# Performance work log

Hardware: AMD Instinct MI355X
Metric: run time of the kernel (lower is better)

## Reference

```python
import jax, jax.numpy as jnp
import numpy as np


def setup_inputs() -> dict:
    key = jax.random.key(0)
    k1, k2 = jax.random.split(key)
    x = jax.random.normal(k1, (16, 2048, 512), dtype=jnp.float32)
    embed = jax.random.normal(k2, (4096, 512), dtype=jnp.float32)
    return {"x": x, "embed": embed}


def reference(x, embed):
    # encode: flatten leading dims, compute -||x - e||^2 via expansion, argmax
    shape = x.shape
    xf = x.reshape(-1, shape[-1])                       # [N, d]
    x_sq = jnp.sum(xf * xf, axis=1, keepdims=True)      # [N, 1]
    e_sq = jnp.sum(embed * embed, axis=1)[None, :]      # [1, K]
    dist = -(x_sq - 2.0 * (xf @ embed.T) + e_sq)        # [N, K]
    embed_ind = jnp.argmax(dist, axis=-1)               # [N]
    embed_ind = embed_ind.reshape(shape[:-1])           # [B, S]
    # decode: embedding lookup (dequantize)
    quantize = embed[embed_ind]                         # [B, S, d]
    return embed_ind, quantize
```

## Files before the change

kernel.cpp:

```cpp
#include <hip/hip_runtime.h>
#include <hip/hip_fp16.h>
#include <stdint.h>


typedef _Float16 f16;
typedef __attribute__((ext_vector_type(4))) _Float16 f16x4;
typedef __attribute__((ext_vector_type(8))) _Float16 f16x8;
typedef __attribute__((ext_vector_type(4))) float f32x4;

#define DDIM 512
#define KCODES 4096
#define NSPLIT 2
#define BM 256
#define BN 256
#define BK 32
#define NCH ((KCODES / NSPLIT) / BN)
#define NSTEPS (NCH * (DDIM / BK))
#define PSTRIDE (NSPLIT * 2)

__device__ __forceinline__ void gload_lds16(const void* g, void* l) {
  __builtin_amdgcn_global_load_lds(
      (const __attribute__((address_space(1))) void*)g,
      (__attribute__((address_space(3))) void*)l,
      16, 0, 0);
}

__global__ void convert_split(const float* __restrict__ in,
                              f16* __restrict__ hi, f16* __restrict__ lo, int n4) {
  int stride = gridDim.x * blockDim.x;
  for (int i = blockIdx.x * blockDim.x + threadIdx.x; i < n4; i += stride) {
    float4 v = ((const float4*)in)[i];
    float vv[4] = {v.x, v.y, v.z, v.w};
    f16x4 h, l;
#pragma unroll
    for (int j = 0; j < 4; ++j) {
      _Float16 hh = (_Float16)vv[j];
      h[j] = hh;
      l[j] = (_Float16)(vv[j] - (float)hh);
    }
    ((f16x4*)hi)[i] = h;
    ((f16x4*)lo)[i] = l;
  }
}

__global__ void esq_kernel(const float* __restrict__ e, float* __restrict__ esq) {
  int gw = (blockIdx.x * blockDim.x + threadIdx.x) >> 6;
  int lane = threadIdx.x & 63;
  if (gw >= KCODES) return;
  const float4* row = (const float4*)(e + (size_t)gw * DDIM);
  float4 a = row[lane * 2];
  float4 b = row[lane * 2 + 1];
  double s = (double)a.x * a.x + (double)a.y * a.y + (double)a.z * a.z + (double)a.w * a.w +
             (double)b.x * b.x + (double)b.y * b.y + (double)b.z * b.z + (double)b.w * b.w;
#pragma unroll
  for (int m = 32; m; m >>= 1) s += __shfl_xor(s, m, 64);
  if (lane == 0) esq[gw] = (float)s;
}

__global__ __launch_bounds__(512, 2) void vq_main(
    const f16* __restrict__ Ah, const f16* __restrict__ Al,
    const f16* __restrict__ Bh, const f16* __restrict__ Bl,
    const float* __restrict__ esq, float2* __restrict__ partials, int nRowBlocks) {
  __shared__ char lds[131072];
  __shared__ float esqLds[KCODES / NSPLIT];

  int nwg = gridDim.x;
  int bid = blockIdx.x;
  int cpx = nwg >> 3;
  int swz = (bid & 7) * cpx + (bid >> 3);
  int nsp = swz / nRowBlocks;
  int brow = swz % nRowBlocks;
  int rowbase = brow * BM;

  int tid = threadIdx.x;
  int lane = tid & 63;
  int wv = tid >> 6;
  int wr = wv >> 1, wc = wv & 1;
  int l15 = lane & 15, lg = lane >> 4;

  const int aoff = (wr * 64 + l15) * 64 + lg * 16;
  const int boff = (wc * 128 + l15) * 64 + lg * 16;

  int srow = tid >> 2;
  int skoff = (tid & 3) * 8;
  const int codesPer = KCODES / NSPLIT;

  const f16* aSrcH = Ah + (size_t)(rowbase + srow) * DDIM + skoff;
  const f16* aSrcL = Al + (size_t)(rowbase + srow) * DDIM + skoff;
  const f16* bBaseH = Bh + (size_t)(nsp * codesPer + srow) * DDIM + skoff;
  const f16* bBaseL = Bl + (size_t)(nsp * codesPer + srow) * DDIM + skoff;

  auto STAGE = [&](int buf, int ch, int kk) {
    char* base = lds + buf * 65536 + wv * 1024;
    size_t bo = (size_t)(ch * BN) * DDIM + kk;
    gload_lds16(aSrcH + kk, base);
    gload_lds16(aSrcH + kk + (size_t)128 * DDIM, base + 8192);
    gload_lds16(aSrcL + kk, base + 16384);
    gload_lds16(aSrcL + kk + (size_t)128 * DDIM, base + 16384 + 8192);
    gload_lds16(bBaseH + bo, base + 32768);
    gload_lds16(bBaseH + bo + (size_t)128 * DDIM, base + 32768 + 8192);
    gload_lds16(bBaseL + bo, base + 49152);
    gload_lds16(bBaseL + bo + (size_t)128 * DDIM, base + 49152 + 8192);
  };

  float bestv[16];
  int besti[16];
#pragma unroll
  for (int t = 0; t < 16; ++t) { bestv[t] = -3.4e38f; besti[t] = 0; }

  f32x4 acc[4][8];

  {
    float4 ev = ((const float4*)(esq + nsp * codesPer))[tid];
    ((float4*)esqLds)[tid] = make_float4(0.5f * ev.x, 0.5f * ev.y, 0.5f * ev.z, 0.5f * ev.w);
  }
  STAGE(0, 0, 0);
  __syncthreads();

#pragma unroll 1
  for (int s = 0; s < NSTEPS; ++s) {
    int cur = s & 1;
    int ch = s >> 4;
    int ns = s + 1;
    if (ns < NSTEPS) {
      STAGE(cur ^ 1, ns >> 4, (ns & 15) * BK);
      asm volatile("s_waitcnt vmcnt(8)" ::: "memory");
    } else {
      asm volatile("s_waitcnt vmcnt(0)" ::: "memory");
    }
    __builtin_amdgcn_s_barrier();
    __builtin_amdgcn_sched_barrier(0);

    if ((s & 15) == 0) {
#pragma unroll
      for (int i = 0; i < 4; ++i)
#pragma unroll
        for (int j = 0; j < 8; ++j) acc[i][j] = (f32x4){0.f, 0.f, 0.f, 0.f};
    }

    char* base = lds + cur * 65536;
    f16x8 ah[4], al[4], bh[8], bl[8];
#pragma unroll
    for (int i = 0; i < 4; ++i) ah[i] = *(const f16x8*)(base + aoff + i * 1024);
#pragma unroll
    for (int j = 0; j < 8; ++j) bh[j] = *(const f16x8*)(base + 32768 + boff + j * 1024);
    __builtin_amdgcn_s_setprio(1);
#pragma unroll
    for (int i = 0; i < 4; ++i)
#pragma unroll
      for (int j = 0; j < 8; ++j)
        acc[i][j] = __builtin_amdgcn_mfma_f32_16x16x32_f16(ah[i], bh[j], acc[i][j], 0, 0, 0);
    __builtin_amdgcn_s_setprio(0);
#pragma unroll
    for (int i = 0; i < 4; ++i) al[i] = *(const f16x8*)(base + 16384 + aoff + i * 1024);
    __builtin_amdgcn_s_setprio(1);
#pragma unroll
    for (int i = 0; i < 4; ++i)
#pragma unroll
      for (int j = 0; j < 8; ++j)
        acc[i][j] = __builtin_amdgcn_mfma_f32_16x16x32_f16(al[i], bh[j], acc[i][j], 0, 0, 0);
    __builtin_amdgcn_s_setprio(0);
#pragma unroll
    for (int j = 0; j < 8; ++j) bl[j] = *(const f16x8*)(base + 49152 + boff + j * 1024);
    __builtin_amdgcn_s_setprio(1);
#pragma unroll
    for (int i = 0; i < 4; ++i)
#pragma unroll
      for (int j = 0; j < 8; ++j)
        acc[i][j] = __builtin_amdgcn_mfma_f32_16x16x32_f16(ah[i], bl[j], acc[i][j], 0, 0, 0);
    __builtin_amdgcn_s_setprio(0);

    if ((s & 15) == 15) {
      int cloc = ch * BN + wc * 128;
#pragma unroll
      for (int j = 0; j < 8; ++j) {
        float eh = esqLds[cloc + j * 16 + l15];
        int code = nsp * codesPer + cloc + j * 16 + l15;
#pragma unroll
        for (int i = 0; i < 4; ++i)
#pragma unroll
          for (int r = 0; r < 4; ++r) {
            float v = acc[i][j][r] - eh;
            int t = i * 4 + r;
            if (v > bestv[t]) { bestv[t] = v; besti[t] = code; }
          }
      }
    }
    __builtin_amdgcn_sched_barrier(0);
    __builtin_amdgcn_s_barrier();
  }

#pragma unroll
  for (int m = 1; m < 16; m <<= 1) {
#pragma unroll
    for (int t = 0; t < 16; ++t) {
      float ov = __shfl_xor(bestv[t], m, 64);
      int oi = __shfl_xor(besti[t], m, 64);
      if (ov > bestv[t] || (ov == bestv[t] && oi < besti[t])) { bestv[t] = ov; besti[t] = oi; }
    }
  }
  if (l15 == 0) {
#pragma unroll
    for (int i = 0; i < 4; ++i)
#pragma unroll
      for (int r = 0; r < 4; ++r) {
        int row = rowbase + wr * 64 + i * 16 + lg * 4 + r;
        partials[(size_t)row * PSTRIDE + nsp * 2 + wc] =
            make_float2(bestv[i * 4 + r], (float)besti[i * 4 + r]);
      }
  }
}

__global__ void reduce_decode(const float* __restrict__ embed,
                              const float2* __restrict__ partials,
                              float* __restrict__ outIdx, float* __restrict__ outQ,
                              int nRows) {
  int gw = (blockIdx.x * blockDim.x + threadIdx.x) >> 6;
  int lane = threadIdx.x & 63;
  if (gw >= nRows) return;
  float bv = -3.4e38f;
  int bi = 0x7fffffff;
#pragma unroll
  for (int s = 0; s < PSTRIDE; ++s) {
    float2 p = partials[(size_t)gw * PSTRIDE + s];
    int idx = (int)p.y;
    if (p.x > bv || (p.x == bv && idx < bi)) { bv = p.x; bi = idx; }
  }
  if (lane == 0) outIdx[gw] = (float)bi;
  const float4* src = (const float4*)(embed + (size_t)bi * DDIM);
  float4* dst = (float4*)(outQ + (size_t)gw * DDIM);
  dst[lane] = src[lane];
  dst[lane + 64] = src[lane + 64];
}

extern "C" void kernel_launch(void* const* d_in, const int* in_sizes, int n_in,
                              void* d_out, int out_size, void* d_ws, size_t ws_size,
                              hipStream_t stream) {
  const float* x = (const float*)d_in[0];
  const float* embed = (const float*)d_in[1];
  int nX = in_sizes[0];
  int nRows = nX / DDIM;
  int nRowBlocks = nRows / BM;

  float* out = (float*)d_out;
  float* outIdx = out;
  float* outQ = out + nRows;

  size_t szA = (size_t)nRows * DDIM * sizeof(f16);
  size_t szB = (size_t)KCODES * DDIM * sizeof(f16);
  size_t szEsq = (size_t)KCODES * sizeof(float);
  size_t szPart = (size_t)nRows * PSTRIDE * sizeof(float2);

  char* ws = (char*)d_ws;
  f16 *Ah, *Al, *Bh, *Bl;
  float* esq;
  float2* parts;
  size_t needFull = 2 * szA + 2 * szB + szEsq + szPart;
  if (ws_size >= needFull) {
    Ah = (f16*)ws;
    Al = (f16*)(ws + szA);
    Bh = (f16*)(ws + 2 * szA);
    Bl = (f16*)(ws + 2 * szA + szB);
    esq = (float*)(ws + 2 * szA + 2 * szB);
    parts = (float2*)(ws + 2 * szA + 2 * szB + szEsq);
  } else {
    Ah = (f16*)outQ;
    Al = Ah + (size_t)nRows * DDIM;
    Bh = (f16*)ws;
    Bl = (f16*)(ws + szB);
    esq = (float*)(ws + 2 * szB);
    parts = (float2*)(ws + 2 * szB + szEsq);
  }

  int n4x = nX / 4;
  int n4e = in_sizes[1] / 4;
  hipLaunchKernelGGL(convert_split, dim3(2048), dim3(256), 0, stream, x, Ah, Al, n4x);
  hipLaunchKernelGGL(convert_split, dim3((n4e + 255) / 256), dim3(256), 0, stream, embed, Bh, Bl, n4e);
  hipLaunchKernelGGL(esq_kernel, dim3(KCODES / 4), dim3(256), 0, stream, embed, esq);
  hipLaunchKernelGGL(vq_main, dim3(nRowBlocks * NSPLIT), dim3(512), 0, stream,
                     Ah, Al, Bh, Bl, esq, parts, nRowBlocks);
  hipLaunchKernelGGL(reduce_decode, dim3(nRows / 4), dim3(256), 0, stream,
                     embed, parts, outIdx, outQ, nRows);
}
```

Baseline: 410.8 us.

## Replace split-fp16 GEMM with single fp16 pass plus exact fixup of ambiguous rows

After: 1.061 ms. +158.2%, slower.

```diff
diff --git a/kernel.cpp b/kernel.cpp
--- a/kernel.cpp
+++ b/kernel.cpp
@@ -13,10 +13,10 @@
 #define NSPLIT 2
 #define BM 256
 #define BN 256
-#define BK 32
 #define NCH ((KCODES / NSPLIT) / BN)
-#define NSTEPS (NCH * (DDIM / BK))
+#define NSTEPS (NCH * (DDIM / 64))
 #define PSTRIDE (NSPLIT * 2)
+#define M_AMBIG 0.15f
 
 __device__ __forceinline__ void gload_lds16(const void* g, void* l) {
   __builtin_amdgcn_global_load_lds(
@@ -25,21 +25,14 @@
       16, 0, 0);
 }
 
-__global__ void convert_split(const float* __restrict__ in,
-                              f16* __restrict__ hi, f16* __restrict__ lo, int n4) {
+__global__ void convert_hi(const float* __restrict__ in, f16* __restrict__ hi, int n4) {
   int stride = gridDim.x * blockDim.x;
   for (int i = blockIdx.x * blockDim.x + threadIdx.x; i < n4; i += stride) {
     float4 v = ((const float4*)in)[i];
-    float vv[4] = {v.x, v.y, v.z, v.w};
-    f16x4 h, l;
-#pragma unroll
-    for (int j = 0; j < 4; ++j) {
-      _Float16 hh = (_Float16)vv[j];
-      h[j] = hh;
-      l[j] = (_Float16)(vv[j] - (float)hh);
-    }
+    f16x4 h;
+    h[0] = (_Float16)v.x; h[1] = (_Float16)v.y;
+    h[2] = (_Float16)v.z; h[3] = (_Float16)v.w;
     ((f16x4*)hi)[i] = h;
-    ((f16x4*)lo)[i] = l;
   }
 }
 
@@ -57,10 +50,11 @@
   if (lane == 0) esq[gw] = (float)s;
 }
 
-__global__ __launch_bounds__(512, 2) void vq_main(
-    const f16* __restrict__ Ah, const f16* __restrict__ Al,
-    const f16* __restrict__ Bh, const f16* __restrict__ Bl,
-    const float* __restrict__ esq, float2* __restrict__ partials, int nRowBlocks) {
+__global__ void zero_counter(int* c) { *c = 0; }
+
+__global__ __launch_bounds__(512, 2) void vq_approx(
+    const f16* __restrict__ Ah, const f16* __restrict__ Bh,
+    const float* __restrict__ esq, float4* __restrict__ partials, int nRowBlocks) {
   __shared__ char lds[131072];
   __shared__ float esqLds[KCODES / NSPLIT];
 
@@ -85,28 +79,26 @@
   int skoff = (tid & 3) * 8;
   const int codesPer = KCODES / NSPLIT;
 
-  const f16* aSrcH = Ah + (size_t)(rowbase + srow) * DDIM + skoff;
-  const f16* aSrcL = Al + (size_t)(rowbase + srow) * DDIM + skoff;
-  const f16* bBaseH = Bh + (size_t)(nsp * codesPer + srow) * DDIM + skoff;
-  const f16* bBaseL = Bl + (size_t)(nsp * codesPer + srow) * DDIM + skoff;
+  const f16* aSrc = Ah + (size_t)(rowbase + srow) * DDIM + skoff;
+  const f16* bBase = Bh + (size_t)(nsp * codesPer + srow) * DDIM + skoff;
 
   auto STAGE = [&](int buf, int ch, int kk) {
     char* base = lds + buf * 65536 + wv * 1024;
     size_t bo = (size_t)(ch * BN) * DDIM + kk;
-    gload_lds16(aSrcH + kk, base);
-    gload_lds16(aSrcH + kk + (size_t)128 * DDIM, base + 8192);
-    gload_lds16(aSrcL + kk, base + 16384);
-    gload_lds16(aSrcL + kk + (size_t)128 * DDIM, base + 16384 + 8192);
-    gload_lds16(bBaseH + bo, base + 32768);
-    gload_lds16(bBaseH + bo + (size_t)128 * DDIM, base + 32768 + 8192);
-    gload_lds16(bBaseL + bo, base + 49152);
-    gload_lds16(bBaseL + bo + (size_t)128 * DDIM, base + 49152 + 8192);
+    gload_lds16(aSrc + kk, base);
+    gload_lds16(aSrc + kk + (size_t)128 * DDIM, base + 8192);
+    gload_lds16(aSrc + kk + 32, base + 16384);
+    gload_lds16(aSrc + kk + 32 + (size_t)128 * DDIM, base + 16384 + 8192);
+    gload_lds16(bBase + bo, base + 32768);
+    gload_lds16(bBase + bo + (size_t)128 * DDIM, base + 32768 + 8192);
+    gload_lds16(bBase + bo + 32, base + 49152);
+    gload_lds16(bBase + bo + 32 + (size_t)128 * DDIM, base + 49152 + 8192);
   };
 
-  float bestv[16];
-  int besti[16];
-#pragma unroll
-  for (int t = 0; t < 16; ++t) { bestv[t] = -3.4e38f; besti[t] = 0; }
+  float v1[16], v2[16];
+  int i1[16];
+#pragma unroll
+  for (int t = 0; t < 16; ++t) { v1[t] = -3.4e38f; v2[t] = -3.4e38f; i1[t] = 0; }
 
   f32x4 acc[4][8];
 
@@ -120,18 +112,11 @@
 #pragma unroll 1
   for (int s = 0; s < NSTEPS; ++s) {
     int cur = s & 1;
-    int ch = s >> 4;
+    int ch = s >> 3;
     int ns = s + 1;
-    if (ns < NSTEPS) {
-      STAGE(cur ^ 1, ns >> 4, (ns & 15) * BK);
-      asm volatile("s_waitcnt vmcnt(8)" ::: "memory");
-    } else {
-      asm volatile("s_waitcnt vmcnt(0)" ::: "memory");
-    }
-    __builtin_amdgcn_s_barrier();
-    __builtin_amdgcn_sched_barrier(0);
-
-    if ((s & 15) == 0) {
+    if (ns < NSTEPS) STAGE(cur ^ 1, ns >> 3, (ns & 7) * 64);
+
+    if ((s & 7) == 0) {
 #pragma unroll
       for (int i = 0; i < 4; ++i)
 #pragma unroll
@@ -139,38 +124,27 @@
     }
 
     char* base = lds + cur * 65536;
-    f16x8 ah[4], al[4], bh[8], bl[8];
-#pragma unroll
-    for (int i = 0; i < 4; ++i) ah[i] = *(const f16x8*)(base + aoff + i * 1024);
-#pragma unroll
-    for (int j = 0; j < 8; ++j) bh[j] = *(const f16x8*)(base + 32768 + boff + j * 1024);
-    __builtin_amdgcn_s_setprio(1);
+    f16x8 af[4], bf[8];
+#pragma unroll
+    for (int i = 0; i < 4; ++i) af[i] = *(const f16x8*)(base + aoff + i * 1024);
+#pragma unroll
+    for (int j = 0; j < 8; ++j) bf[j] = *(const f16x8*)(base + 32768 + boff + j * 1024);
 #pragma unroll
     for (int i = 0; i < 4; ++i)
 #pragma unroll
       for (int j = 0; j < 8; ++j)
-        acc[i][j] = __builtin_amdgcn_mfma_f32_16x16x32_f16(ah[i], bh[j], acc[i][j], 0, 0, 0);
-    __builtin_amdgcn_s_setprio(0);
-#pragma unroll
-    for (int i = 0; i < 4; ++i) al[i] = *(const f16x8*)(base + 16384 + aoff + i * 1024);
-    __builtin_amdgcn_s_setprio(1);
+        acc[i][j] = __builtin_amdgcn_mfma_f32_16x16x32_f16(af[i], bf[j], acc[i][j], 0, 0, 0);
+#pragma unroll
+    for (int i = 0; i < 4; ++i) af[i] = *(const f16x8*)(base + 16384 + aoff + i * 1024);
+#pragma unroll
+    for (int j = 0; j < 8; ++j) bf[j] = *(const f16x8*)(base + 49152 + boff + j * 1024);
 #pragma unroll
     for (int i = 0; i < 4; ++i)
 #pragma unroll
       for (int j = 0; j < 8; ++j)
-        acc[i][j] = __builtin_amdgcn_mfma_f32_16x16x32_f16(al[i], bh[j], acc[i][j], 0, 0, 0);
-    __builtin_amdgcn_s_setprio(0);
-#pragma unroll
-    for (int j = 0; j < 8; ++j) bl[j] = *(const f16x8*)(base + 49152 + boff + j * 1024);
-    __builtin_amdgcn_s_setprio(1);
-#pragma unroll
-    for (int i = 0; i < 4; ++i)
-#pragma unroll
-      for (int j = 0; j < 8; ++j)
-        acc[i][j] = __builtin_amdgcn_mfma_f32_16x16x32_f16(ah[i], bl[j], acc[i][j], 0, 0, 0);
-    __builtin_amdgcn_s_setprio(0);
-
-    if ((s & 15) == 15) {
+        acc[i][j] = __builtin_amdgcn_mfma_f32_16x16x32_f16(af[i], bf[j], acc[i][j], 0, 0, 0);
+
+    if ((s & 7) == 7) {
       int cloc = ch * BN + wc * 128;
 #pragma unroll
       for (int j = 0; j < 8; ++j) {
@@ -182,21 +156,27 @@
           for (int r = 0; r < 4; ++r) {
             float v = acc[i][j][r] - eh;
             int t = i * 4 + r;
-            if (v > bestv[t]) { bestv[t] = v; besti[t] = code; }
+            if (v > v1[t]) { v2[t] = v1[t]; v1[t] = v; i1[t] = code; }
+            else if (v > v2[t]) v2[t] = v;
           }
       }
     }
-    __builtin_amdgcn_sched_barrier(0);
-    __builtin_amdgcn_s_barrier();
+    __syncthreads();
   }
 
 #pragma unroll
   for (int m = 1; m < 16; m <<= 1) {
 #pragma unroll
     for (int t = 0; t < 16; ++t) {
-      float ov = __shfl_xor(bestv[t], m, 64);
-      int oi = __shfl_xor(besti[t], m, 64);
-      if (ov > bestv[t] || (ov == bestv[t] && oi < besti[t])) { bestv[t] = ov; besti[t] = oi; }
+      float ov1 = __shfl_xor(v1[t], m, 64);
+      int oi1 = __shfl_xor(i1[t], m, 64);
+      float ov2 = __shfl_xor(v2[t], m, 64);
+      if (ov1 > v1[t] || (ov1 == v1[t] && oi1 < i1[t])) {
+        v2[t] = fmaxf(v1[t], ov2);
+        v1[t] = ov1; i1[t] = oi1;
+      } else {
+        v2[t] = fmaxf(v2[t], ov1);
+      }
     }
   }
   if (l15 == 0) {
@@ -205,28 +185,92 @@
 #pragma unroll
       for (int r = 0; r < 4; ++r) {
         int row = rowbase + wr * 64 + i * 16 + lg * 4 + r;
+        int t = i * 4 + r;
         partials[(size_t)row * PSTRIDE + nsp * 2 + wc] =
-            make_float2(bestv[i * 4 + r], (float)besti[i * 4 + r]);
-      }
-  }
-}
-
-__global__ void reduce_decode(const float* __restrict__ embed,
-                              const float2* __restrict__ partials,
-                              float* __restrict__ outIdx, float* __restrict__ outQ,
-                              int nRows) {
+            make_float4(v1[t], (float)i1[t], v2[t], 0.f);
+      }
+  }
+}
+
+__global__ void reduce_ambig(const float4* __restrict__ partials,
+                             float* __restrict__ outIdx,
+                             int* __restrict__ counter, int* __restrict__ list,
+                             int nRows) {
+  int row = blockIdx.x * blockDim.x + threadIdx.x;
+  if (row >= nRows) return;
+  float v1 = -3.4e38f, v2 = -3.4e38f;
+  int i1 = 0x7fffffff;
+#pragma unroll
+  for (int s = 0; s < PSTRIDE; ++s) {
+    float4 p = partials[(size_t)row * PSTRIDE + s];
+    int pi = (int)p.y;
+    if (p.x > v1 || (p.x == v1 && pi < i1)) {
+      v2 = fmaxf(v1, p.z);
+      v1 = p.x; i1 = pi;
+    } else {
+      v2 = fmaxf(v2, p.x);
+    }
+  }
+  outIdx[row] = (float)i1;
+  if (v1 - v2 <= M_AMBIG) {
+    int pos = atomicAdd(counter, 1);
+    list[pos] = row;
+  }
+}
+
+__global__ __launch_bounds__(256) void fixup_exact(
+    const float* __restrict__ x, const float* __restrict__ embed,
+    const int* __restrict__ counter, const int* __restrict__ list,
+    float* __restrict__ outIdx) {
+  __shared__ float xr[DDIM];
+  __shared__ double sv[256];
+  __shared__ int si[256];
+  int tid = threadIdx.x;
+  int cnt = *counter;
+  for (int w = blockIdx.x; w < cnt; w += gridDim.x) {
+    int row = list[w];
+    for (int t = tid; t < DDIM; t += 256) xr[t] = x[(size_t)row * DDIM + t];
+    __syncthreads();
+    double best = -1e300;
+    int bidx = 0;
+#pragma unroll 1
+    for (int j = 0; j < KCODES / 256; ++j) {
+      int c = tid + j * 256;
+      const float4* e4 = (const float4*)(embed + (size_t)c * DDIM);
+      const float4* x4 = (const float4*)xr;
+      double s = 0.0;
+#pragma unroll 4
+      for (int k = 0; k < DDIM / 4; ++k) {
+        float4 ev = e4[k];
+        float4 xv = x4[k];
+        s += ((double)xv.x - 0.5 * (double)ev.x) * (double)ev.x;
+        s += ((double)xv.y - 0.5 * (double)ev.y) * (double)ev.y;
+        s += ((double)xv.z - 0.5 * (double)ev.z) * (double)ev.z;
+        s += ((double)xv.w - 0.5 * (double)ev.w) * (double)ev.w;
+      }
+      if (s > best || (s == best && c < bidx)) { best = s; bidx = c; }
+    }
+    sv[tid] = best; si[tid] = bidx;
+    __syncthreads();
+    for (int m = 128; m; m >>= 1) {
+      if (tid < m) {
+        if (sv[tid + m] > sv[tid] || (sv[tid + m] == sv[tid] && si[tid + m] < si[tid])) {
+          sv[tid] = sv[tid + m]; si[tid] = si[tid + m];
+        }
+      }
+      __syncthreads();
+    }
+    if (tid == 0) outIdx[row] = (float)si[0];
+    __syncthreads();
+  }
+}
+
+__global__ void decode(const float* __restrict__ embed, const float* __restrict__ outIdx,
+                       float* __restrict__ outQ, int nRows) {
   int gw = (blockIdx.x * blockDim.x + threadIdx.x) >> 6;
   int lane = threadIdx.x & 63;
   if (gw >= nRows) return;
-  float bv = -3.4e38f;
-  int bi = 0x7fffffff;
-#pragma unroll
-  for (int s = 0; s < PSTRIDE; ++s) {
-    float2 p = partials[(size_t)gw * PSTRIDE + s];
-    int idx = (int)p.y;
-    if (p.x > bv || (p.x == bv && idx < bi)) { bv = p.x; bi = idx; }
-  }
-  if (lane == 0) outIdx[gw] = (float)bi;
+  int bi = (int)outIdx[gw];
   const float4* src = (const float4*)(embed + (size_t)bi * DDIM);
   float4* dst = (float4*)(outQ + (size_t)gw * DDIM);
   dst[lane] = src[lane];
@@ -249,36 +293,44 @@
   size_t szA = (size_t)nRows * DDIM * sizeof(f16);
   size_t szB = (size_t)KCODES * DDIM * sizeof(f16);
   size_t szEsq = (size_t)KCODES * sizeof(float);
-  size_t szPart = (size_t)nRows * PSTRIDE * sizeof(float2);
+  size_t szPart = (size_t)nRows * PSTRIDE * sizeof(float4);
+  size_t szList = (size_t)nRows * sizeof(int);
 
   char* ws = (char*)d_ws;
-  f16 *Ah, *Al, *Bh, *Bl;
+  f16 *Ah, *Bh;
   float* esq;
-  float2* parts;
-  size_t needFull = 2 * szA + 2 * szB + szEsq + szPart;
+  float4* parts;
+  int* counter;
+  int* list;
+  size_t needFull = szA + szB + szEsq + szPart + szList + 256;
   if (ws_size >= needFull) {
     Ah = (f16*)ws;
-    Al = (f16*)(ws + szA);
-    Bh = (f16*)(ws + 2 * szA);
-    Bl = (f16*)(ws + 2 * szA + szB);
-    esq = (float*)(ws + 2 * szA + 2 * szB);
-    parts = (float2*)(ws + 2 * szA + 2 * szB + szEsq);
+    Bh = (f16*)(ws + szA);
+    esq = (float*)(ws + szA + szB);
+    parts = (float4*)(ws + szA + szB + szEsq);
+    list = (int*)(ws + szA + szB + szEsq + szPart);
+    counter = (int*)(ws + szA + szB + szEsq + szPart + szList);
   } else {
     Ah = (f16*)outQ;
-    Al = Ah + (size_t)nRows * DDIM;
     Bh = (f16*)ws;
-    Bl = (f16*)(ws + szB);
-    esq = (float*)(ws + 2 * szB);
-    parts = (float2*)(ws + 2 * szB + szEsq);
+    esq = (float*)(ws + szB);
+    parts = (float4*)(ws + szB + szEsq);
+    list = (int*)(ws + szB + szEsq + szPart);
+    counter = (int*)(ws + szB + szEsq + szPart + szList);
   }
 
   int n4x = nX / 4;
   int n4e = in_sizes[1] / 4;
-  hipLaunchKernelGGL(convert_split, dim3(2048), dim3(256), 0, stream, x, Ah, Al, n4x);
-  hipLaunchKernelGGL(convert_split, dim3((n4e + 255) / 256), dim3(256), 0, stream, embed, Bh, Bl, n4e);
+  hipLaunchKernelGGL(convert_hi, dim3(2048), dim3(256), 0, stream, x, Ah, n4x);
+  hipLaunchKernelGGL(convert_hi, dim3((n4e + 255) / 256), dim3(256), 0, stream, embed, Bh, n4e);
   hipLaunchKernelGGL(esq_kernel, dim3(KCODES / 4), dim3(256), 0, stream, embed, esq);
-  hipLaunchKernelGGL(vq_main, dim3(nRowBlocks * NSPLIT), dim3(512), 0, stream,
-                     Ah, Al, Bh, Bl, esq, parts, nRowBlocks);
-  hipLaunchKernelGGL(reduce_decode, dim3(nRows / 4), dim3(256), 0, stream,
-                     embed, parts, outIdx, outQ, nRows);
-}
+  hipLaunchKernelGGL(zero_counter, dim3(1), dim3(1), 0, stream, counter);
+  hipLaunchKernelGGL(vq_approx, dim3(nRowBlocks * NSPLIT), dim3(512), 0, stream,
+                     Ah, Bh, esq, parts, nRowBlocks);
+  hipLaunchKernelGGL(reduce_ambig, dim3(nRows / 256), dim3(256), 0, stream,
+                     parts, outIdx, counter, list, nRows);
+  hipLaunchKernelGGL(fixup_exact, dim3(256), dim3(256), 0, stream,
+                     x, embed, counter, list, outIdx);
+  hipLaunchKernelGGL(decode, dim3(nRows / 4), dim3(256), 0, stream,
+                     embed, outIdx, outQ, nRows);
+}
```
